# Optimization experiments

Measured on AMD Instinct MI355X. Metric: run time of the kernel, lower is better.

The kernel has to match this reference:

```python
import jax, jax.numpy as jnp
import numpy as np

D_MODEL = 1024
N_HEADS = 16
HEAD_DIM = D_MODEL // N_HEADS
B, T = 4, 2048


def setup_inputs() -> dict:
    key = jax.random.key(0)
    k_x, k_qw, k_qb, k_ow, k_ob = jax.random.split(key, 5)
    x = jax.random.normal(k_x, (B, T, D_MODEL), dtype=jnp.float32)
    # torch nn.Linear weights: [out_features, in_features]
    s = 1.0 / np.sqrt(D_MODEL)
    qkv_w = jax.random.uniform(k_qw, (3 * D_MODEL, D_MODEL), jnp.float32, -s, s)
    qkv_b = jax.random.uniform(k_qb, (3 * D_MODEL,), jnp.float32, -s, s)
    out_w = jax.random.uniform(k_ow, (D_MODEL, D_MODEL), jnp.float32, -s, s)
    out_b = jax.random.uniform(k_ob, (D_MODEL,), jnp.float32, -s, s)
    mask = jnp.tril(jnp.ones((T, T), dtype=jnp.int32))[None, None]  # [1,1,T,T] causal
    return {"x": x, "qkv_w": qkv_w, "qkv_b": qkv_b, "out_w": out_w, "out_b": out_b, "mask": mask}


def reference(x, qkv_w, qkv_b, out_w, out_b, mask):
    Bs, Ts, C = x.shape
    qkv = x @ qkv_w.T + qkv_b  # [B,T,3C]
    q, k, v = jnp.split(qkv, 3, axis=-1)
    # [B,T,C] -> [B,H,T,Dh]
    def heads(t):
        return t.reshape(Bs, Ts, N_HEADS, HEAD_DIM).transpose(0, 2, 1, 3)
    q, k, v = heads(q), heads(k), heads(v)
    scale = 1.0 / np.sqrt(HEAD_DIM).astype(np.float32)
    attn = jnp.einsum('bhqd,bhkd->bhqk', q, k) * scale  # [B,H,T,T]
    attn = jnp.where(mask == 0, jnp.finfo(attn.dtype).min, attn)
    attn = jax.nn.softmax(attn, axis=-1)
    y = jnp.einsum('bhqk,bhkd->bhqd', attn, v)  # [B,H,T,Dh]
    y = y.transpose(0, 2, 1, 3).reshape(Bs, Ts, C)
    return y @ out_w.T + out_b
```

## Files before the change

### kernel.cpp

```cpp
#include <hip/hip_runtime.h>
#include <hip/hip_bf16.h>
#include <stdint.h>

#define BB 4
#define TT 2048
#define CC 1024
#define HH 16
#define DH 64
#define MM (BB*TT)
#define NQKV (3*CC)

typedef __attribute__((ext_vector_type(8))) short bf16x8;
typedef __attribute__((ext_vector_type(4))) float f32x4;

#define GLL16(g, l) __builtin_amdgcn_global_load_lds( \
  (const __attribute__((address_space(1))) unsigned int*)(g), \
  (__attribute__((address_space(3))) unsigned int*)(l), 16, 0, 0)

__device__ inline unsigned short f2b(float f) {
  __hip_bfloat16 h = __float2bfloat16(f);
  return *reinterpret_cast<unsigned short*>(&h);
}

__global__ __launch_bounds__(256) void cvt3(
    const float* __restrict__ a, int na, unsigned short* __restrict__ da,
    const float* __restrict__ b, int nb, unsigned short* __restrict__ db,
    const float* __restrict__ c, int nc, unsigned short* __restrict__ dc) {
  const int stride = gridDim.x * 256 * 4;
  const int base = (blockIdx.x * 256 + threadIdx.x) * 4;
  for (int i = base; i < na; i += stride) {
    float4 v = *reinterpret_cast<const float4*>(a + i);
    ushort4 o; o.x = f2b(v.x); o.y = f2b(v.y); o.z = f2b(v.z); o.w = f2b(v.w);
    *reinterpret_cast<ushort4*>(da + i) = o;
  }
  for (int i = base; i < nb; i += stride) {
    float4 v = *reinterpret_cast<const float4*>(b + i);
    ushort4 o; o.x = f2b(v.x); o.y = f2b(v.y); o.z = f2b(v.z); o.w = f2b(v.w);
    *reinterpret_cast<ushort4*>(db + i) = o;
  }
  for (int i = base; i < nc; i += stride) {
    float4 v = *reinterpret_cast<const float4*>(c + i);
    ushort4 o; o.x = f2b(v.x); o.y = f2b(v.y); o.z = f2b(v.z); o.w = f2b(v.w);
    *reinterpret_cast<ushort4*>(dc + i) = o;
  }
}

__global__ __launch_bounds__(256) void gemm_qkv(
    const unsigned short* __restrict__ A, const unsigned short* __restrict__ Bt,
    const float* __restrict__ bias,
    unsigned short* __restrict__ qd, unsigned short* __restrict__ kd,
    unsigned short* __restrict__ vtd) {
  __shared__ alignas(16) unsigned short sA[128 * 32];
  __shared__ alignas(16) unsigned short sB[128 * 32];
  const int tid = threadIdx.x;
  const int lane = tid & 63, wid = tid >> 6;
  const int wr = wid >> 1, wc = wid & 1;
  const int lrow = lane & 15, lgrp = lane >> 4;
  const int lk = lgrp * 8;
  const int bn0 = blockIdx.x * 128, bm0 = blockIdx.y * 128;
  f32x4 acc[4][4] = {};
  for (int kt = 0; kt < 1024; kt += 32) {
#pragma unroll
    for (int j = 0; j < 2; ++j) {
      int c = j * 256 + tid;
      const unsigned short* ga = A  + (size_t)(bm0 + (c >> 2)) * 1024 + kt + (c & 3) * 8;
      const unsigned short* gb = Bt + (size_t)(bn0 + (c >> 2)) * 1024 + kt + (c & 3) * 8;
      GLL16(ga, (char*)sA + j * 4096 + wid * 1024);
      GLL16(gb, (char*)sB + j * 4096 + wid * 1024);
    }
    __syncthreads();
    bf16x8 af[4], bfr[4];
#pragma unroll
    for (int mm = 0; mm < 4; ++mm)
      af[mm] = *reinterpret_cast<const bf16x8*>(&sA[(wr * 64 + mm * 16 + lrow) * 32 + lk]);
#pragma unroll
    for (int nn = 0; nn < 4; ++nn)
      bfr[nn] = *reinterpret_cast<const bf16x8*>(&sB[(wc * 64 + nn * 16 + lrow) * 32 + lk]);
#pragma unroll
    for (int mm = 0; mm < 4; ++mm)
#pragma unroll
      for (int nn = 0; nn < 4; ++nn)
        acc[mm][nn] = __builtin_amdgcn_mfma_f32_16x16x32_bf16(af[mm], bfr[nn], acc[mm][nn], 0, 0, 0);
    __syncthreads();
  }
  const int part = bn0 >> 10;
#pragma unroll
  for (int mm = 0; mm < 4; ++mm)
#pragma unroll
    for (int nn = 0; nn < 4; ++nn) {
      const int col = bn0 + wc * 64 + nn * 16 + lrow;
      const int cc = col & 1023;
      const int h = cc >> 6, dd = cc & 63;
      const float bv = bias[col];
#pragma unroll
      for (int r = 0; r < 4; ++r) {
        const int row = bm0 + wr * 64 + mm * 16 + lgrp * 4 + r;
        const int b = row >> 11, t = row & 2047;
        float v = acc[mm][nn][r] + bv;
        const size_t bh = (size_t)(b * HH + h);
        if (part == 0)      qd[(bh * TT + t) * DH + dd] = f2b(v * 0.125f);
        else if (part == 1) kd[(bh * TT + t) * DH + dd] = f2b(v);
        else {
          const int tp = (t & ~63) | ((t & 15) << 2) | ((t >> 4) & 3);
          vtd[(bh * DH + dd) * TT + tp] = f2b(v);
        }
      }
    }
}

__device__ __attribute__((always_inline)) inline void stage_chunk(
    const unsigned short* kb, const unsigned short* vb, int kv0,
    char* sK, char* sV, int tid, int wid) {
  const int row = tid >> 3;
  const int col = (tid & 7) * 16;
  const int scol = col ^ ((row & 7) << 4);
  GLL16((const char*)kb + (size_t)(kv0 + row) * 128 + scol, sK + wid * 1024);
  GLL16((const char*)vb + (size_t)row * (TT * 2) + (size_t)kv0 * 2 + scol, sV + wid * 1024);
}

__device__ __attribute__((always_inline)) inline void tile_step(
    const bf16x8& qf0, const bf16x8& qf1, f32x4 (&o)[4], float (&m)[4], float (&lp)[4],
    const char* cK, const char* cV, char* sP, int kv0, int r0, bool diag,
    int lrow, int lgrp) {
  f32x4 s[4];
  __builtin_amdgcn_s_setprio(1);
#pragma unroll
  for (int f = 0; f < 4; ++f) {
    const int key = f * 16 + lrow;
    const char* kr = cK + key * 128;
    const int sw = (key & 7) << 4;
    bf16x8 kf0 = *(const bf16x8*)(kr + ((lgrp * 16) ^ sw));
    bf16x8 kf1 = *(const bf16x8*)(kr + ((64 + lgrp * 16) ^ sw));
    f32x4 z = {};
    z = __builtin_amdgcn_mfma_f32_16x16x32_bf16(qf0, kf0, z, 0, 0, 0);
    s[f] = __builtin_amdgcn_mfma_f32_16x16x32_bf16(qf1, kf1, z, 0, 0, 0);
  }
  __builtin_amdgcn_s_setprio(0);
#pragma unroll
  for (int r = 0; r < 4; ++r) {
    const int qrow = r0 + lgrp * 4 + r;
    float v0 = s[0][r], v1 = s[1][r], v2 = s[2][r], v3 = s[3][r];
    if (diag) {
      v0 = (kv0 +      lrow <= qrow) ? v0 : -1e30f;
      v1 = (kv0 + 16 + lrow <= qrow) ? v1 : -1e30f;
      v2 = (kv0 + 32 + lrow <= qrow) ? v2 : -1e30f;
      v3 = (kv0 + 48 + lrow <= qrow) ? v3 : -1e30f;
    }
    float mx = fmaxf(fmaxf(v0, v1), fmaxf(v2, v3));
#pragma unroll
    for (int off = 8; off; off >>= 1) mx = fmaxf(mx, __shfl_xor(mx, off, 64));
    const float mn = fmaxf(m[r], mx);
    const float alpha = __expf(m[r] - mn);
    const float p0 = __expf(v0 - mn), p1 = __expf(v1 - mn);
    const float p2 = __expf(v2 - mn), p3 = __expf(v3 - mn);
    lp[r] = lp[r] * alpha + (p0 + p1) + (p2 + p3);
    m[r] = mn;
#pragma unroll
    for (int nn = 0; nn < 4; ++nn) o[nn][r] *= alpha;
    const int rw = lgrp * 4 + r;
    const int rb = rw * 128;
    const int sw = (rw & 7) << 4;
    ushort4 pk;
    pk.x = f2b(p0); pk.y = f2b(p1); pk.z = f2b(p2); pk.w = f2b(p3);
    *(ushort4*)(sP + rb + ((lrow * 8) ^ sw)) = pk;
  }
  const int prb = lrow * 128;
  const int psw = (lrow & 7) << 4;
  bf16x8 pf0 = *(const bf16x8*)(sP + prb + ((lgrp * 16) ^ psw));
  bf16x8 pf1 = *(const bf16x8*)(sP + prb + ((64 + lgrp * 16) ^ psw));
  __builtin_amdgcn_s_setprio(1);
#pragma unroll
  for (int nn = 0; nn < 4; ++nn) {
    const int d = nn * 16 + lrow;
    const char* vr = cV + d * 128;
    const int vsw = (d & 7) << 4;
    bf16x8 vf0 = *(const bf16x8*)(vr + ((lgrp * 16) ^ vsw));
    bf16x8 vf1 = *(const bf16x8*)(vr + ((64 + lgrp * 16) ^ vsw));
    o[nn] = __builtin_amdgcn_mfma_f32_16x16x32_bf16(pf0, vf0, o[nn], 0, 0, 0);
    o[nn] = __builtin_amdgcn_mfma_f32_16x16x32_bf16(pf1, vf1, o[nn], 0, 0, 0);
  }
  __builtin_amdgcn_s_setprio(0);
}

__device__ __attribute__((always_inline)) inline void store_frag(
    unsigned short* __restrict__ outb, const f32x4 (&o)[4], const float (&lp)[4],
    int b, int h, int r0, int lrow, int lgrp) {
#pragma unroll
  for (int r = 0; r < 4; ++r) {
    float t = lp[r];
#pragma unroll
    for (int off = 8; off; off >>= 1) t += __shfl_xor(t, off, 64);
    const float inv = 1.f / t;
    const int qrow = r0 + lgrp * 4 + r;
#pragma unroll
    for (int nn = 0; nn < 4; ++nn)
      outb[((size_t)(b * TT + qrow)) * CC + h * DH + nn * 16 + lrow] = f2b(o[nn][r] * inv);
  }
}

__global__ __launch_bounds__(512, 2) void attn_k(
    const unsigned short* __restrict__ q, const unsigned short* __restrict__ k,
    const unsigned short* __restrict__ vt, unsigned short* __restrict__ outb) {
  const int tid = threadIdx.x;
  const int lane = tid & 63, wid = tid >> 6;
  const int lrow = lane & 15, lgrp = lane >> 4;
  const int bid = blockIdx.x;
  const int bh = bid >> 3;
  const int pr = bid & 7;
  const int b = bh >> 4, h = bh & 15;
  const int qt_lo = pr, qt_hi = 15 - pr;
  const int n_ch = 2 * (qt_hi + 1);
  const int lo_last = 2 * qt_lo + 1;

  __shared__ alignas(16) char smem[65536];
  char* sK = smem;
  char* sV = smem + 24576;
  char* sP = smem + 49152 + wid * 2048;

  const unsigned short* qb = q + (size_t)bh * TT * DH;
  const unsigned short* kb = k + (size_t)bh * TT * DH;
  const unsigned short* vb = vt + (size_t)bh * DH * TT;

  const int r0_lo = qt_lo * 128 + wid * 16;
  const int r0_hi = qt_hi * 128 + wid * 16;

  bf16x8 qlo0 = *(const bf16x8*)&qb[(size_t)(r0_lo + lrow) * DH + lgrp * 8];
  bf16x8 qlo1 = *(const bf16x8*)&qb[(size_t)(r0_lo + lrow) * DH + 32 + lgrp * 8];
  bf16x8 qhi0 = *(const bf16x8*)&qb[(size_t)(r0_hi + lrow) * DH + lgrp * 8];
  bf16x8 qhi1 = *(const bf16x8*)&qb[(size_t)(r0_hi + lrow) * DH + 32 + lgrp * 8];

  f32x4 olo[4] = {}, ohi[4] = {};
  float mlo[4], llo[4], mhi[4], lhi[4];
#pragma unroll
  for (int r = 0; r < 4; ++r) { mlo[r] = -1e30f; llo[r] = 0.f; mhi[r] = -1e30f; lhi[r] = 0.f; }

  stage_chunk(kb, vb, 0,  sK,        sV,        tid, wid);
  stage_chunk(kb, vb, 64, sK + 8192, sV + 8192, tid, wid);
  asm volatile("s_waitcnt vmcnt(2)" ::: "memory");
  __builtin_amdgcn_s_barrier();

  int cur = 0;
  for (int ci = 0; ci < n_ch; ++ci) {
    const bool pre = (ci + 2 < n_ch);
    if (pre) {
      const int pb = cur == 0 ? 2 : cur - 1;
      stage_chunk(kb, vb, (ci + 2) * 64, sK + pb * 8192, sV + pb * 8192, tid, wid);
    }
    const char* cK = sK + cur * 8192;
    const char* cV = sV + cur * 8192;
    const int kv0 = ci * 64;
    if (ci <= lo_last)
      tile_step(qlo0, qlo1, olo, mlo, llo, cK, cV, sP, kv0, r0_lo, kv0 + 63 > r0_lo, lrow, lgrp);
    tile_step(qhi0, qhi1, ohi, mhi, lhi, cK, cV, sP, kv0, r0_hi, kv0 + 63 > r0_hi, lrow, lgrp);
    if (pre) { asm volatile("s_waitcnt vmcnt(2)" ::: "memory"); }
    else     { asm volatile("s_waitcnt vmcnt(0)" ::: "memory"); }
    __builtin_amdgcn_s_barrier();
    cur = cur == 2 ? 0 : cur + 1;
  }

  store_frag(outb, olo, llo, b, h, r0_lo, lrow, lgrp);
  store_frag(outb, ohi, lhi, b, h, r0_hi, lrow, lgrp);
}

__global__ __launch_bounds__(256) void gemm_proj(
    const unsigned short* __restrict__ A, const unsigned short* __restrict__ Bt,
    const float* __restrict__ bias, float* __restrict__ out) {
  __shared__ alignas(16) unsigned short sA[128 * 32];
  __shared__ alignas(16) unsigned short sB[128 * 32];
  const int tid = threadIdx.x;
  const int lane = tid & 63, wid = tid >> 6;
  const int wr = wid >> 1, wc = wid & 1;
  const int lrow = lane & 15, lgrp = lane >> 4;
  const int lk = lgrp * 8;
  const int bn0 = blockIdx.x * 128, bm0 = blockIdx.y * 128;
  f32x4 acc[4][4] = {};
  for (int kt = 0; kt < 1024; kt += 32) {
#pragma unroll
    for (int j = 0; j < 2; ++j) {
      int c = j * 256 + tid;
      const unsigned short* ga = A  + (size_t)(bm0 + (c >> 2)) * 1024 + kt + (c & 3) * 8;
      const unsigned short* gb = Bt + (size_t)(bn0 + (c >> 2)) * 1024 + kt + (c & 3) * 8;
      GLL16(ga, (char*)sA + j * 4096 + wid * 1024);
      GLL16(gb, (char*)sB + j * 4096 + wid * 1024);
    }
    __syncthreads();
    bf16x8 af[4], bfr[4];
#pragma unroll
    for (int mm = 0; mm < 4; ++mm)
      af[mm] = *reinterpret_cast<const bf16x8*>(&sA[(wr * 64 + mm * 16 + lrow) * 32 + lk]);
#pragma unroll
    for (int nn = 0; nn < 4; ++nn)
      bfr[nn] = *reinterpret_cast<const bf16x8*>(&sB[(wc * 64 + nn * 16 + lrow) * 32 + lk]);
#pragma unroll
    for (int mm = 0; mm < 4; ++mm)
#pragma unroll
      for (int nn = 0; nn < 4; ++nn)
        acc[mm][nn] = __builtin_amdgcn_mfma_f32_16x16x32_bf16(af[mm], bfr[nn], acc[mm][nn], 0, 0, 0);
    __syncthreads();
  }
#pragma unroll
  for (int mm = 0; mm < 4; ++mm)
#pragma unroll
    for (int nn = 0; nn < 4; ++nn) {
      const int col = bn0 + wc * 64 + nn * 16 + lrow;
      const float bv = bias[col];
#pragma unroll
      for (int r = 0; r < 4; ++r) {
        const int row = bm0 + wr * 64 + mm * 16 + lgrp * 4 + r;
        out[(size_t)row * 1024 + col] = acc[mm][nn][r] + bv;
      }
    }
}

extern "C" void kernel_launch(void* const* d_in, const int* in_sizes, int n_in,
                              void* d_out, int out_size, void* d_ws, size_t ws_size,
                              hipStream_t stream) {
  const float* x     = (const float*)d_in[0];
  const float* qkv_w = (const float*)d_in[1];
  const float* qkv_b = (const float*)d_in[2];
  const float* out_w = (const float*)d_in[3];
  const float* out_b = (const float*)d_in[4];
  float* out = (float*)d_out;
  char* ws = (char*)d_ws;

  unsigned short* xb  = (unsigned short*)(ws);
  unsigned short* att = (unsigned short*)(ws);
  unsigned short* wq  = (unsigned short*)(ws + 16777216);
  unsigned short* wo  = (unsigned short*)(ws + 23068672);
  unsigned short* qd  = (unsigned short*)(ws + 25165824);
  unsigned short* kd  = (unsigned short*)(ws + 41943040);
  unsigned short* vtd = (unsigned short*)(ws + 58720256);

  cvt3<<<2048, 256, 0, stream>>>(x, MM * CC, xb,
                                 qkv_w, NQKV * CC, wq,
                                 out_w, CC * CC, wo);

  gemm_qkv<<<dim3(NQKV / 128, MM / 128), 256, 0, stream>>>(xb, wq, qkv_b, qd, kd, vtd);
  attn_k<<<BB * HH * 8, 512, 0, stream>>>(qd, kd, vtd, att);
  gemm_proj<<<dim3(CC / 128, MM / 128), 256, 0, stream>>>(att, wo, out_b, out);
}
```

Before: 250.8 us.

## Triple-buffer GEMM LDS loads and fold log2e into Q scale for exp2

Both GEMM kernels move from one LDS buffer with two barriers per k-step to a three-stage ring. Tiles are prefetched two steps ahead with global_load_lds, and manual vmcnt waits leave one barrier per step, so global-load latency can overlap with MFMA work. Separately, the Q scale now includes log2(e), which lets the attention softmax use exp2f instead of __expf. The cost is triple the LDS use per GEMM block (48KB), which may lower occupancy.

```diff
diff --git a/kernel.cpp b/kernel.cpp
--- a/kernel.cpp
+++ b/kernel.cpp
@@ -45,13 +45,26 @@
   }
 }
 
+__device__ __attribute__((always_inline)) inline void gemm_stage(
+    const unsigned short* __restrict__ A, const unsigned short* __restrict__ Bt,
+    int bm0, int bn0, int kt, char* sAb, char* sBb, int tid, int wid) {
+#pragma unroll
+  for (int j = 0; j < 2; ++j) {
+    int c = j * 256 + tid;
+    const unsigned short* ga = A  + (size_t)(bm0 + (c >> 2)) * 1024 + kt + (c & 3) * 8;
+    const unsigned short* gb = Bt + (size_t)(bn0 + (c >> 2)) * 1024 + kt + (c & 3) * 8;
+    GLL16(ga, sAb + j * 4096 + wid * 1024);
+    GLL16(gb, sBb + j * 4096 + wid * 1024);
+  }
+}
+
 __global__ __launch_bounds__(256) void gemm_qkv(
     const unsigned short* __restrict__ A, const unsigned short* __restrict__ Bt,
     const float* __restrict__ bias,
     unsigned short* __restrict__ qd, unsigned short* __restrict__ kd,
     unsigned short* __restrict__ vtd) {
-  __shared__ alignas(16) unsigned short sA[128 * 32];
-  __shared__ alignas(16) unsigned short sB[128 * 32];
+  __shared__ alignas(16) char sA[3 * 8192];
+  __shared__ alignas(16) char sB[3 * 8192];
   const int tid = threadIdx.x;
   const int lane = tid & 63, wid = tid >> 6;
   const int wr = wid >> 1, wc = wid & 1;
@@ -59,30 +72,38 @@
   const int lk = lgrp * 8;
   const int bn0 = blockIdx.x * 128, bm0 = blockIdx.y * 128;
   f32x4 acc[4][4] = {};
-  for (int kt = 0; kt < 1024; kt += 32) {
-#pragma unroll
-    for (int j = 0; j < 2; ++j) {
-      int c = j * 256 + tid;
-      const unsigned short* ga = A  + (size_t)(bm0 + (c >> 2)) * 1024 + kt + (c & 3) * 8;
-      const unsigned short* gb = Bt + (size_t)(bn0 + (c >> 2)) * 1024 + kt + (c & 3) * 8;
-      GLL16(ga, (char*)sA + j * 4096 + wid * 1024);
-      GLL16(gb, (char*)sB + j * 4096 + wid * 1024);
-    }
-    __syncthreads();
+
+  gemm_stage(A, Bt, bm0, bn0, 0,  sA,        sB,        tid, wid);
+  gemm_stage(A, Bt, bm0, bn0, 32, sA + 8192, sB + 8192, tid, wid);
+  asm volatile("s_waitcnt vmcnt(4)" ::: "memory");
+  __builtin_amdgcn_s_barrier();
+
+  int cur = 0;
+  for (int t = 0; t < 32; ++t) {
+    if (t + 2 < 32) {
+      const int pb = cur == 0 ? 2 : cur - 1;
+      gemm_stage(A, Bt, bm0, bn0, (t + 2) * 32, sA + pb * 8192, sB + pb * 8192, tid, wid);
+    }
+    const unsigned short* cA = (const unsigned short*)(sA + cur * 8192);
+    const unsigned short* cB = (const unsigned short*)(sB + cur * 8192);
     bf16x8 af[4], bfr[4];
 #pragma unroll
     for (int mm = 0; mm < 4; ++mm)
-      af[mm] = *reinterpret_cast<const bf16x8*>(&sA[(wr * 64 + mm * 16 + lrow) * 32 + lk]);
+      af[mm] = *reinterpret_cast<const bf16x8*>(&cA[(wr * 64 + mm * 16 + lrow) * 32 + lk]);
 #pragma unroll
     for (int nn = 0; nn < 4; ++nn)
-      bfr[nn] = *reinterpret_cast<const bf16x8*>(&sB[(wc * 64 + nn * 16 + lrow) * 32 + lk]);
+      bfr[nn] = *reinterpret_cast<const bf16x8*>(&cB[(wc * 64 + nn * 16 + lrow) * 32 + lk]);
 #pragma unroll
     for (int mm = 0; mm < 4; ++mm)
 #pragma unroll
       for (int nn = 0; nn < 4; ++nn)
         acc[mm][nn] = __builtin_amdgcn_mfma_f32_16x16x32_bf16(af[mm], bfr[nn], acc[mm][nn], 0, 0, 0);
-    __syncthreads();
-  }
+    if (t + 2 < 32) { asm volatile("s_waitcnt vmcnt(4)" ::: "memory"); }
+    else            { asm volatile("s_waitcnt vmcnt(0)" ::: "memory"); }
+    __builtin_amdgcn_s_barrier();
+    cur = cur == 2 ? 0 : cur + 1;
+  }
+
   const int part = bn0 >> 10;
 #pragma unroll
   for (int mm = 0; mm < 4; ++mm)
@@ -98,7 +119,7 @@
         const int b = row >> 11, t = row & 2047;
         float v = acc[mm][nn][r] + bv;
         const size_t bh = (size_t)(b * HH + h);
-        if (part == 0)      qd[(bh * TT + t) * DH + dd] = f2b(v * 0.125f);
+        if (part == 0)      qd[(bh * TT + t) * DH + dd] = f2b(v * 0.18033688011112042f);
         else if (part == 1) kd[(bh * TT + t) * DH + dd] = f2b(v);
         else {
           const int tp = (t & ~63) | ((t & 15) << 2) | ((t >> 4) & 3);
@@ -150,9 +171,9 @@
 #pragma unroll
     for (int off = 8; off; off >>= 1) mx = fmaxf(mx, __shfl_xor(mx, off, 64));
     const float mn = fmaxf(m[r], mx);
-    const float alpha = __expf(m[r] - mn);
-    const float p0 = __expf(v0 - mn), p1 = __expf(v1 - mn);
-    const float p2 = __expf(v2 - mn), p3 = __expf(v3 - mn);
+    const float alpha = exp2f(m[r] - mn);
+    const float p0 = exp2f(v0 - mn), p1 = exp2f(v1 - mn);
+    const float p2 = exp2f(v2 - mn), p3 = exp2f(v3 - mn);
     lp[r] = lp[r] * alpha + (p0 + p1) + (p2 + p3);
     m[r] = mn;
 #pragma unroll
@@ -265,8 +286,8 @@
 __global__ __launch_bounds__(256) void gemm_proj(
     const unsigned short* __restrict__ A, const unsigned short* __restrict__ Bt,
     const float* __restrict__ bias, float* __restrict__ out) {
-  __shared__ alignas(16) unsigned short sA[128 * 32];
-  __shared__ alignas(16) unsigned short sB[128 * 32];
+  __shared__ alignas(16) char sA[3 * 8192];
+  __shared__ alignas(16) char sB[3 * 8192];
   const int tid = threadIdx.x;
   const int lane = tid & 63, wid = tid >> 6;
   const int wr = wid >> 1, wc = wid & 1;
@@ -274,30 +295,38 @@
   const int lk = lgrp * 8;
   const int bn0 = blockIdx.x * 128, bm0 = blockIdx.y * 128;
   f32x4 acc[4][4] = {};
-  for (int kt = 0; kt < 1024; kt += 32) {
-#pragma unroll
-    for (int j = 0; j < 2; ++j) {
-      int c = j * 256 + tid;
-      const unsigned short* ga = A  + (size_t)(bm0 + (c >> 2)) * 1024 + kt + (c & 3) * 8;
-      const unsigned short* gb = Bt + (size_t)(bn0 + (c >> 2)) * 1024 + kt + (c & 3) * 8;
-      GLL16(ga, (char*)sA + j * 4096 + wid * 1024);
-      GLL16(gb, (char*)sB + j * 4096 + wid * 1024);
-    }
-    __syncthreads();
+
+  gemm_stage(A, Bt, bm0, bn0, 0,  sA,        sB,        tid, wid);
+  gemm_stage(A, Bt, bm0, bn0, 32, sA + 8192, sB + 8192, tid, wid);
+  asm volatile("s_waitcnt vmcnt(4)" ::: "memory");
+  __builtin_amdgcn_s_barrier();
+
+  int cur = 0;
+  for (int t = 0; t < 32; ++t) {
+    if (t + 2 < 32) {
+      const int pb = cur == 0 ? 2 : cur - 1;
+      gemm_stage(A, Bt, bm0, bn0, (t + 2) * 32, sA + pb * 8192, sB + pb * 8192, tid, wid);
+    }
+    const unsigned short* cA = (const unsigned short*)(sA + cur * 8192);
+    const unsigned short* cB = (const unsigned short*)(sB + cur * 8192);
     bf16x8 af[4], bfr[4];
 #pragma unroll
     for (int mm = 0; mm < 4; ++mm)
-      af[mm] = *reinterpret_cast<const bf16x8*>(&sA[(wr * 64 + mm * 16 + lrow) * 32 + lk]);
+      af[mm] = *reinterpret_cast<const bf16x8*>(&cA[(wr * 64 + mm * 16 + lrow) * 32 + lk]);
 #pragma unroll
     for (int nn = 0; nn < 4; ++nn)
-      bfr[nn] = *reinterpret_cast<const bf16x8*>(&sB[(wc * 64 + nn * 16 + lrow) * 32 + lk]);
+      bfr[nn] = *reinterpret_cast<const bf16x8*>(&cB[(wc * 64 + nn * 16 + lrow) * 32 + lk]);
 #pragma unroll
     for (int mm = 0; mm < 4; ++mm)
 #pragma unroll
       for (int nn = 0; nn < 4; ++nn)
         acc[mm][nn] = __builtin_amdgcn_mfma_f32_16x16x32_bf16(af[mm], bfr[nn], acc[mm][nn], 0, 0, 0);
-    __syncthreads();
-  }
+    if (t + 2 < 32) { asm volatile("s_waitcnt vmcnt(4)" ::: "memory"); }
+    else            { asm volatile("s_waitcnt vmcnt(0)" ::: "memory"); }
+    __builtin_amdgcn_s_barrier();
+    cur = cur == 2 ? 0 : cur + 1;
+  }
+
 #pragma unroll
   for (int mm = 0; mm < 4; ++mm)
 #pragma unroll
```

Measured after the change: 273.6 us. +9.1%, slower.
